# Optimization experiments

Measured on AMD Instinct MI355X. Metric: run time of the kernel, lower is better.

Reference implementation:

```python
import jax, jax.numpy as jnp
import numpy as np

D = 384      # d_model
DM = 256     # memory feature dim
DF = 1536    # dim_feedforward
EPS = 1e-5


def _layer_norm(x, g, b):
    m = jnp.mean(x, axis=-1, keepdims=True)
    v = jnp.mean(jnp.square(x - m), axis=-1, keepdims=True)
    return (x - m) * jax.lax.rsqrt(v + EPS) * g + b


def setup_inputs() -> dict:
    key = jax.random.key(0)
    ks = jax.random.split(key, 24)
    B, T, T1, Tc = 8, 2048, 2048, 2048
    s = 0.02
    inp = {
        "tgt": jax.random.normal(ks[0], (B, T, D), jnp.float32),
        "memory": jax.random.normal(ks[1], (B, T1, DM), jnp.float32),
        "a1": jnp.float32(0.5),
        "score_c": jax.random.normal(ks[2], (B, 1, Tc, T1), jnp.float32) * 0.1,
        "out_c": jax.random.normal(ks[3], (B, Tc, D), jnp.float32),
        # attention projections
        "Wq": jax.random.normal(ks[4], (D, D), jnp.float32) * s,
        "bq": jnp.zeros((D,), jnp.float32),
        "Wk": jax.random.normal(ks[5], (DM, D), jnp.float32) * s,
        "bk": jnp.zeros((D,), jnp.float32),
        "Wv": jax.random.normal(ks[6], (DM, D), jnp.float32) * s,
        "bv": jnp.zeros((D,), jnp.float32),
        "Wu": jax.random.normal(ks[7], (D, D), jnp.float32) * s,  # unknown
        "bu": jnp.zeros((D,), jnp.float32),
        "Wn": jax.random.normal(ks[8], (D, D), jnp.float32) * s,  # known
        "bn": jnp.zeros((D,), jnp.float32),
        # FFN
        "W1": jax.random.normal(ks[9], (D, DF), jnp.float32) * s,
        "b1": jnp.zeros((DF,), jnp.float32),
        "W2": jax.random.normal(ks[10], (DF, D), jnp.float32) * s,
        "b2": jnp.zeros((D,), jnp.float32),
        # LayerNorms
        "g1": jnp.ones((D,), jnp.float32),
        "be1": jnp.zeros((D,), jnp.float32),
        "g2": jnp.ones((D,), jnp.float32),
        "be2": jnp.zeros((D,), jnp.float32),
    }
    return inp


def reference(tgt, memory, a1, score_c, out_c,
              Wq, bq, Wk, bk, Wv, bv, Wu, bu, Wn, bn,
              W1, b1, W2, b2, g1, be1, g2, be2):
    # --- En_De_Attention (n_head = 1; dropout p=0 / eval mode -> identity) ---
    scale = 1.0 / jnp.sqrt(jnp.float32(D))
    q = tgt @ Wq + bq                  # [B,T,D]
    k = memory @ Wk + bk               # [B,T1,D]
    v = memory @ Wv + bv               # [B,T1,D]
    att = jnp.einsum('btd,bsd->bts', q, k) * scale            # [B,T,T1]

    unknow = tgt @ Wu + bu             # [B,T,D]
    know = out_c @ Wn + bn             # [B,Tc,D]
    score1 = jnp.einsum('btd,bcd->btc', unknow, know) * scale  # [B,T,Tc]
    mixed = jnp.einsum('btc,bcs->bts', score1, score_c[:, 0])  # [B,T,T1]

    # tt = a1 in (0,1]: blended-score branch of the original module
    score = a1 * jax.nn.softmax(mixed, axis=-1) \
          + (1.0 - a1) * jax.nn.softmax(att, axis=-1)          # [B,T,T1]
    z = jnp.einsum('bts,bsd->btd', score, v)                   # [B,T,D]

    # --- residual + norm1 ---
    x = _layer_norm(tgt + z, g1, be1)
    # --- FFN (relu) + residual + norm2 (dropout eval -> identity) ---
    ff = jax.nn.relu(x @ W1 + b1) @ W2 + b2
    out = _layer_norm(x + ff, g2, be2)
    # score2 returned with head dim, matching torch shape [B,1,T,T1]
    return out, score[:, None]
```

## Files before the change

### kernel.cpp

```cpp
#include <hip/hip_runtime.h>
#include <stdint.h>

typedef __attribute__((ext_vector_type(8))) short bf16x8;
typedef __attribute__((ext_vector_type(4))) float f32x4;

__device__ __forceinline__ short f2bf(float f) {
    union { float f; unsigned u; } v; v.f = f;
    unsigned r = v.u + 0x7fffu + ((v.u >> 16) & 1u);
    return (short)(r >> 16);
}
__device__ __forceinline__ float bf2f(short s) {
    union { unsigned u; float f; } v;
    v.u = ((unsigned)(unsigned short)s) << 16;
    return v.f;
}

__device__ __forceinline__ void gld16(const void* g, void* l) {
    auto gp = reinterpret_cast<const __attribute__((address_space(1))) unsigned int*>(
        reinterpret_cast<uintptr_t>(g));
    auto lp = reinterpret_cast<__attribute__((address_space(3))) unsigned int*>(
        reinterpret_cast<uintptr_t>(l));
    __builtin_amdgcn_global_load_lds(gp, lp, 16, 0, 0);
}

template<int OUTBF, int BIASMODE , int DORELU>
__global__ __launch_bounds__(256, 2) void gemmWide(
    const short* __restrict__ Ag, const short* __restrict__ Bg,
    void* __restrict__ Cg, const float* __restrict__ bias,
    int K, int lda, int ldb, int ldc,
    long long sA, long long sB, long long sC,
    long long dA, long long dB, long long dC, float scale)
{
    __shared__ short lds[3 * 12288];
    const int t = threadIdx.x;
    const int lane = t & 63;
    const int wave = t >> 6;
    const int wm = wave >> 1, wn = wave & 1;

    const int gx = gridDim.x, gy = gridDim.y;
    const int nwg = gx * gy * gridDim.z;
    int id = blockIdx.x + gx * (blockIdx.y + gy * blockIdx.z);
    id = (id & 7) * (nwg >> 3) + (id >> 3);
    const int bx = id % gx;
    const int by = (id / gx) % gy;
    const int bz = id / (gx * gy);
    const int zlo = bz & 7, zhi = bz >> 3;

    const long long row0 = (long long)by * 128;
    const long long col0 = (long long)bx * 256;
    const int NT = K >> 5;

    const int gk = ((t & 3) ^ ((t >> 2) & 3) ^ ((t >> 4) & 3)) * 8;
    const short* Asrc = Ag + zlo * sA + zhi * dA + (row0 + (t >> 2)) * (long long)lda + gk;
    const short* Bsrc = Bg + zlo * sB + zhi * dB + (col0 + (t >> 2)) * (long long)ldb + gk;

    const int frow = lane & 15;
    const int fcol = ((lane >> 4) ^ (frow & 3) ^ ((frow >> 2) & 3)) * 8;

    f32x4 acc[4][8] = {};

#define STG(BUF, KC) do { \
        gld16(Asrc + (KC), &lds[(BUF) * 12288 + t * 8]); \
        gld16(Asrc + (KC) + 64LL * lda, &lds[(BUF) * 12288 + 2048 + t * 8]); \
        gld16(Bsrc + (KC), &lds[(BUF) * 12288 + 4096 + t * 8]); \
        gld16(Bsrc + (KC) + 64LL * ldb, &lds[(BUF) * 12288 + 6144 + t * 8]); \
        gld16(Bsrc + (KC) + 128LL * ldb, &lds[(BUF) * 12288 + 8192 + t * 8]); \
        gld16(Bsrc + (KC) + 192LL * ldb, &lds[(BUF) * 12288 + 10240 + t * 8]); } while (0)

    STG(0, 0);
    STG(1, 32);
    asm volatile("s_waitcnt vmcnt(6)\ns_barrier" ::: "memory");

    for (int kt = 0; kt < NT; ++kt) {
        const int rb = (kt % 3) * 12288;
        bf16x8 av[4], bv[8];
#pragma unroll
        for (int m = 0; m < 4; ++m)
            av[m] = *(const bf16x8*)&lds[rb + (wm * 64 + m * 16 + frow) * 32 + fcol];
#pragma unroll
        for (int n = 0; n < 8; ++n)
            bv[n] = *(const bf16x8*)&lds[rb + 4096 + (wn * 128 + n * 16 + frow) * 32 + fcol];
        if (kt + 2 < NT) STG((kt + 2) % 3, (long long)(kt + 2) * 32);
        __builtin_amdgcn_s_setprio(1);
#pragma unroll
        for (int m = 0; m < 4; ++m)
#pragma unroll
            for (int n = 0; n < 8; ++n)
                acc[m][n] = __builtin_amdgcn_mfma_f32_16x16x32_bf16(av[m], bv[n], acc[m][n], 0, 0, 0);
        __builtin_amdgcn_s_setprio(0);
        if (kt + 1 < NT) {
            if (kt + 2 < NT) asm volatile("s_waitcnt vmcnt(6)\ns_barrier" ::: "memory");
            else             asm volatile("s_waitcnt vmcnt(0)\ns_barrier" ::: "memory");
        }
    }
#undef STG

    const int crow = (lane >> 4) * 4;
    const int ccol = lane & 15;
    const long long cz = zlo * sC + zhi * dC;
#pragma unroll
    for (int m = 0; m < 4; ++m)
#pragma unroll
        for (int n = 0; n < 8; ++n)
#pragma unroll
            for (int i = 0; i < 4; ++i) {
                long long r = row0 + wm * 64 + m * 16 + crow + i;
                long long c = col0 + wn * 128 + n * 16 + ccol;
                float v = acc[m][n][i] * scale;
                if (BIASMODE == 1) v += bias[c];
                if (DORELU) v = fmaxf(v, 0.0f);
                long long idx = cz + r * (long long)ldc + c;
                if (OUTBF) ((short*)Cg)[idx] = f2bf(v);
                else ((float*)Cg)[idx] = v;
            }
}

template<int OUTBF, int BIASMODE , int DORELU>
__global__ __launch_bounds__(256, 3) void gemm128r(
    const short* __restrict__ Ag, const short* __restrict__ Bg,
    void* __restrict__ Cg, const float* __restrict__ bias,
    int K, int lda, int ldb, int ldc,
    long long sA, long long sB, long long sC,
    long long dA, long long dB, long long dC, float scale)
{
    __shared__ short lds[3 * 8192];
    const int t = threadIdx.x;
    const int lane = t & 63;
    const int wave = t >> 6;
    const int wm = wave >> 1, wn = wave & 1;

    const int gx = gridDim.x, gy = gridDim.y;
    const int nwg = gx * gy * gridDim.z;
    int id = blockIdx.x + gx * (blockIdx.y + gy * blockIdx.z);
    id = (id & 7) * (nwg >> 3) + (id >> 3);
    const int bx = id % gx;
    const int by = (id / gx) % gy;
    const int bz = id / (gx * gy);
    const int zlo = bz & 7, zhi = bz >> 3;

    const long long row0 = (long long)by * 128;
    const long long col0 = (long long)bx * 128;
    const int NT = K >> 5;

    const int gk = ((t & 3) ^ ((t >> 2) & 3) ^ ((t >> 4) & 3)) * 8;
    const short* Asrc = Ag + zlo * sA + zhi * dA + (row0 + (t >> 2)) * (long long)lda + gk;
    const short* Bsrc = Bg + zlo * sB + zhi * dB + (col0 + (t >> 2)) * (long long)ldb + gk;

    const int frow = lane & 15;
    const int fcol = ((lane >> 4) ^ (frow & 3) ^ ((frow >> 2) & 3)) * 8;

    f32x4 acc[4][4] = {};

#define STG(BUF, KC) do { \
        gld16(Asrc + (KC), &lds[(BUF) * 8192 + t * 8]); \
        gld16(Asrc + (KC) + 64LL * lda, &lds[(BUF) * 8192 + 2048 + t * 8]); \
        gld16(Bsrc + (KC), &lds[(BUF) * 8192 + 4096 + t * 8]); \
        gld16(Bsrc + (KC) + 64LL * ldb, &lds[(BUF) * 8192 + 6144 + t * 8]); } while (0)

    STG(0, 0);
    STG(1, 32);
    asm volatile("s_waitcnt vmcnt(4)\ns_barrier" ::: "memory");

    for (int kt = 0; kt < NT; ++kt) {
        const int rb = (kt % 3) * 8192;
        bf16x8 av[4], bv[4];
#pragma unroll
        for (int m = 0; m < 4; ++m)
            av[m] = *(const bf16x8*)&lds[rb + (wm * 64 + m * 16 + frow) * 32 + fcol];
#pragma unroll
        for (int n = 0; n < 4; ++n)
            bv[n] = *(const bf16x8*)&lds[rb + 4096 + (wn * 64 + n * 16 + frow) * 32 + fcol];
        if (kt + 2 < NT) STG((kt + 2) % 3, (long long)(kt + 2) * 32);
        __builtin_amdgcn_s_setprio(1);
#pragma unroll
        for (int m = 0; m < 4; ++m)
#pragma unroll
            for (int n = 0; n < 4; ++n)
                acc[m][n] = __builtin_amdgcn_mfma_f32_16x16x32_bf16(av[m], bv[n], acc[m][n], 0, 0, 0);
        __builtin_amdgcn_s_setprio(0);
        if (kt + 1 < NT) {
            if (kt + 2 < NT) asm volatile("s_waitcnt vmcnt(4)\ns_barrier" ::: "memory");
            else             asm volatile("s_waitcnt vmcnt(0)\ns_barrier" ::: "memory");
        }
    }
#undef STG

    const int crow = (lane >> 4) * 4;
    const int ccol = lane & 15;
    const long long cz = zlo * sC + zhi * dC;
#pragma unroll
    for (int m = 0; m < 4; ++m)
#pragma unroll
        for (int n = 0; n < 4; ++n)
#pragma unroll
            for (int i = 0; i < 4; ++i) {
                long long r = row0 + wm * 64 + m * 16 + crow + i;
                long long c = col0 + wn * 64 + n * 16 + ccol;
                float v = acc[m][n][i] * scale;
                if (BIASMODE == 1) v += bias[c];
                if (BIASMODE == 2) v += bias[r];
                if (DORELU) v = fmaxf(v, 0.0f);
                long long idx = cz + r * (long long)ldc + c;
                if (OUTBF) ((short*)Cg)[idx] = f2bf(v);
                else ((float*)Cg)[idx] = v;
            }
}

#define RD_A(RB, M, KS) (*(const bf16x8*)&lds[(RB) + (wm * 64 + (M) * 16 + frow) * 64 + \
        ((((KS) << 2) | fq) ^ (frow & 7)) * 8])
#define RD_B(RB, Nn, KS) (*(const bf16x8*)&lds[(RB) + 8192 + (wn * 64 + (Nn) * 16 + frow) * 64 + \
        ((((KS) << 2) | fq) ^ (frow & 7)) * 8])

__global__ __launch_bounds__(256, 2) void gemm128pz(
    const short* __restrict__ A1, const short* __restrict__ B1, short* __restrict__ C1,
    const float* __restrict__ bias1, int K1, int lda1, int ldb1, int ldc1,
    long long sB1, long long sC1,
    const short* __restrict__ A2, const short* __restrict__ B2, short* __restrict__ C2,
    const float* __restrict__ bias2, int K2, int lda2, int ldb2, int ldc2,
    long long sB2, long long sC2)
{
    __shared__ short lds[2 * 16384];
    const int t = threadIdx.x;
    const int lane = t & 63;
    const int wave = t >> 6;
    const int wm = wave >> 1, wn = wave & 1;

    const int gx = gridDim.x, gy = gridDim.y;
    const int nwg = gx * gy * gridDim.z;
    int id = blockIdx.x + gx * (blockIdx.y + gy * blockIdx.z);
    id = (id & 7) * (nwg >> 3) + (id >> 3);
    const int bx = id % gx;
    const int by = (id / gx) % gy;
    const int bz = id / (gx * gy);

    const bool sel = bz >= 8;
    const int zz = bz & 7;
    const short* Ag = sel ? A2 : A1;
    const short* Bg = sel ? B2 : B1;
    short* Cg = sel ? C2 : C1;
    const float* bias = sel ? bias2 : bias1;
    const int K = sel ? K2 : K1;
    const int lda = sel ? lda2 : lda1;
    const int ldb = sel ? ldb2 : ldb1;
    const int ldc = sel ? ldc2 : ldc1;
    const long long sB = sel ? sB2 : sB1;
    const long long sC = sel ? sC2 : sC1;

    const long long row0 = (long long)by * 128;
    const long long col0 = (long long)bx * 128;
    const int NT = K >> 6;

    const int srow = t >> 3;
    const int gk = ((t & 7) ^ (srow & 7)) * 8;
    const short* Asrc = Ag + (row0 + srow) * (long long)lda + gk;
    const short* Bsrc = Bg + (long long)zz * sB + (col0 + srow) * (long long)ldb + gk;

    const int frow = lane & 15;
    const int fq = lane >> 4;

    f32x4 acc[4][4] = {};

#define STAGE_A(WB, KC) do { _Pragma("unroll") \
        for (int r = 0; r < 4; ++r) \
            gld16(Asrc + (KC) + (long long)r * 32 * lda, &lds[(WB) + t * 8 + r * 2048]); } while (0)
#define STAGE_B(WB, KC) do { _Pragma("unroll") \
        for (int r = 0; r < 4; ++r) \
            gld16(Bsrc + (KC) + (long long)r * 32 * ldb, &lds[(WB) + 8192 + t * 8 + r * 2048]); } while (0)

    STAGE_A(0, 0);
    STAGE_B(0, 0);
    asm volatile("s_waitcnt vmcnt(0)\ns_barrier" ::: "memory");

    for (int kt = 0; kt < NT; ++kt) {
        const int rb = (kt & 1) << 14;
        const int wb = ((kt + 1) & 1) << 14;
        const bool st = (kt + 1) < NT;
        const long long kc = (long long)(kt + 1) << 6;

        bf16x8 av[4], bv[4];

#pragma unroll
        for (int m = 0; m < 4; ++m) av[m] = RD_A(rb, m, 0);
#pragma unroll
        for (int n = 0; n < 4; ++n) bv[n] = RD_B(rb, n, 0);
        if (st) STAGE_A(wb, kc);
        asm volatile("s_barrier" ::: "memory");
        __builtin_amdgcn_s_setprio(1);
#pragma unroll
        for (int m = 0; m < 4; ++m)
#pragma unroll
            for (int n = 0; n < 4; ++n)
                acc[m][n] = __builtin_amdgcn_mfma_f32_16x16x32_bf16(av[m], bv[n], acc[m][n], 0, 0, 0);
        __builtin_amdgcn_s_setprio(0);
        asm volatile("s_barrier" ::: "memory");

#pragma unroll
        for (int m = 0; m < 4; ++m) av[m] = RD_A(rb, m, 1);
#pragma unroll
        for (int n = 0; n < 4; ++n) bv[n] = RD_B(rb, n, 1);
        if (st) STAGE_B(wb, kc);
        asm volatile("s_barrier" ::: "memory");
        __builtin_amdgcn_s_setprio(1);
#pragma unroll
        for (int m = 0; m < 4; ++m)
#pragma unroll
            for (int n = 0; n < 4; ++n)
                acc[m][n] = __builtin_amdgcn_mfma_f32_16x16x32_bf16(av[m], bv[n], acc[m][n], 0, 0, 0);
        __builtin_amdgcn_s_setprio(0);
        if (st) asm volatile("s_waitcnt vmcnt(0)\ns_barrier" ::: "memory");
        else    asm volatile("s_barrier" ::: "memory");
    }
#undef STAGE_A
#undef STAGE_B

    const int crow = (lane >> 4) * 4;
    const int ccol = lane & 15;
    const long long cz = (long long)zz * sC;
#pragma unroll
    for (int m = 0; m < 4; ++m)
#pragma unroll
        for (int n = 0; n < 4; ++n)
#pragma unroll
            for (int i = 0; i < 4; ++i) {
                long long r = row0 + wm * 64 + m * 16 + crow + i;
                long long c = col0 + wn * 64 + n * 16 + ccol;
                float v = acc[m][n][i] + bias[r];
                Cg[cz + r * (long long)ldc + c] = f2bf(v);
            }
}
#undef RD_A
#undef RD_B

__global__ __launch_bounds__(256) void cast_all(
    const float* __restrict__ tgt, const float* __restrict__ mem, const float* __restrict__ outc,
    const float* __restrict__ bq, const float* __restrict__ bu,
    short* __restrict__ tgtb, short* __restrict__ memb, short* __restrict__ outcb,
    float* __restrict__ qubias)
{
    const long long R1 = 1572864;
    const long long R2 = R1 + 1048576;
    const long long R3 = R2 + 1572864;
    const long long R4 = R3 + 192;
    long long i = (long long)blockIdx.x * 256 + threadIdx.x;
    const float* in; short* out; long long j;
    if (i < R1) { in = tgt; out = tgtb; j = i; }
    else if (i < R2) { in = mem; out = memb; j = i - R1; }
    else if (i < R3) { in = outc; out = outcb; j = i - R2; }
    else if (i < R4) {
        j = i - R3;
        ((float4*)qubias)[j] = (j < 96) ? ((const float4*)bq)[j] : ((const float4*)bu)[j - 96];
        return;
    } else return;
    float4 v = ((const float4*)in)[j];
    short4 o;
    o.x = f2bf(v.x); o.y = f2bf(v.y); o.z = f2bf(v.z); o.w = f2bf(v.w);
    ((short4*)out)[j] = o;
}

__global__ __launch_bounds__(256) void transpose_all(
    const float* __restrict__ Wq, const float* __restrict__ Wk, const float* __restrict__ Wv,
    const float* __restrict__ Wu, const float* __restrict__ Wn,
    const float* __restrict__ W1, const float* __restrict__ W2,
    short* __restrict__ WquT, short* __restrict__ WkT, short* __restrict__ WvT,
    short* __restrict__ WnT, short* __restrict__ W1T, short* __restrict__ W2T)
{
    __shared__ float tile[64][65];
    int b = blockIdx.x;
    const float* in; short* out; int R, C, local;
    if (b < 36)       { in = Wq; out = WquT;          R = 384;  C = 384;  local = b; }
    else if (b < 60)  { in = Wk; out = WkT;           R = 256;  C = 384;  local = b - 36; }
    else if (b < 84)  { in = Wv; out = WvT;           R = 256;  C = 384;  local = b - 60; }
    else if (b < 120) { in = Wu; out = WquT + 147456; R = 384;  C = 384;  local = b - 84; }
    else if (b < 156) { in = Wn; out = WnT;           R = 384;  C = 384;  local = b - 120; }
    else if (b < 300) { in = W1; out = W1T;           R = 384;  C = 1536; local = b - 156; }
    else              { in = W2; out = W2T;           R = 1536; C = 384;  local = b - 300; }
    const int nbx = C >> 6;
    const int r0 = (local / nbx) * 64, c0 = (local % nbx) * 64;
    const int lr = threadIdx.x >> 6, lc = threadIdx.x & 63;
#pragma unroll
    for (int i = 0; i < 16; ++i) {
        int r = lr * 16 + i;
        tile[r][lc] = in[(long long)(r0 + r) * C + c0 + lc];
    }
    __syncthreads();
#pragma unroll
    for (int i = 0; i < 16; ++i) {
        int r = lr * 16 + i;
        out[(long long)(c0 + r) * R + r0 + lc] = f2bf(tile[lc][r]);
    }
}

__global__ __launch_bounds__(256) void transpose_cast(
    const float* __restrict__ in, short* __restrict__ out,
    int R, int C, long long sIn, long long sOut)
{
    __shared__ float tile[64][65];
    const long long zi = (long long)blockIdx.z * sIn;
    const long long zo = (long long)blockIdx.z * sOut;
    const int r0 = blockIdx.y * 64, c0 = blockIdx.x * 64;
    const int lr = threadIdx.x >> 6, lc = threadIdx.x & 63;
#pragma unroll
    for (int i = 0; i < 16; ++i) {
        int r = lr * 16 + i;
        tile[r][lc] = in[zi + (long long)(r0 + r) * C + c0 + lc];
    }
    __syncthreads();
#pragma unroll
    for (int i = 0; i < 16; ++i) {
        int r = lr * 16 + i;
        out[zo + (long long)(c0 + r) * R + r0 + lc] = f2bf(tile[lc][r]);
    }
}

__global__ __launch_bounds__(256) void softmax_blend(
    const short* __restrict__ attb, const short* __restrict__ mixb,
    const float* __restrict__ a1p,
    float* __restrict__ outF, short* __restrict__ outB)
{
    const int S = 2048;
    const long long row = blockIdx.x;
    const short* ar = attb + row * S;
    const short* mr = mixb + row * S;
    const int t = threadIdx.x;
    const int wave = t >> 6;

    bf16x8 a8 = *(const bf16x8*)&ar[t * 8];
    bf16x8 m8 = *(const bf16x8*)&mr[t * 8];
    float av[8], mv[8];
#pragma unroll
    for (int i = 0; i < 8; ++i) { av[i] = bf2f(a8[i]); mv[i] = bf2f(m8[i]); }

    float amax = av[0], mmax = mv[0];
#pragma unroll
    for (int i = 1; i < 8; ++i) { amax = fmaxf(amax, av[i]); mmax = fmaxf(mmax, mv[i]); }
#pragma unroll
    for (int o = 32; o; o >>= 1) {
        amax = fmaxf(amax, __shfl_xor(amax, o));
        mmax = fmaxf(mmax, __shfl_xor(mmax, o));
    }
    __shared__ float red[2][4];
    if ((t & 63) == 0) { red[0][wave] = amax; red[1][wave] = mmax; }
    __syncthreads();
    amax = fmaxf(fmaxf(red[0][0], red[0][1]), fmaxf(red[0][2], red[0][3]));
    mmax = fmaxf(fmaxf(red[1][0], red[1][1]), fmaxf(red[1][2], red[1][3]));

    float asum = 0.f, msum = 0.f;
#pragma unroll
    for (int i = 0; i < 8; ++i) {
        av[i] = __expf(av[i] - amax); asum += av[i];
        mv[i] = __expf(mv[i] - mmax); msum += mv[i];
    }
#pragma unroll
    for (int o = 32; o; o >>= 1) {
        asum += __shfl_xor(asum, o);
        msum += __shfl_xor(msum, o);
    }
    __shared__ float red2[2][4];
    if ((t & 63) == 0) { red2[0][wave] = asum; red2[1][wave] = msum; }
    __syncthreads();
    asum = red2[0][0] + red2[0][1] + red2[0][2] + red2[0][3];
    msum = red2[1][0] + red2[1][1] + red2[1][2] + red2[1][3];

    const float a1 = a1p[0];
    const float wm = a1 / msum;
    const float wa = (1.0f - a1) / asum;

    float o0[8];
    bf16x8 ob;
#pragma unroll
    for (int i = 0; i < 8; ++i) {
        float s = wm * mv[i] + wa * av[i];
        o0[i] = s;
        ob[i] = f2bf(s);
    }
    float4 f0, f1;
    f0.x = o0[0]; f0.y = o0[1]; f0.z = o0[2]; f0.w = o0[3];
    f1.x = o0[4]; f1.y = o0[5]; f1.z = o0[6]; f1.w = o0[7];
    *(float4*)&outF[row * S + t * 8] = f0;
    *(float4*)&outF[row * S + t * 8 + 4] = f1;
    *(bf16x8*)&outB[row * S + t * 8] = ob;
}

template<int WRITE_BF, int TWO_Y>
__global__ __launch_bounds__(256) void ln_kernel(
    const float* __restrict__ X, const float* __restrict__ Yr,
    const float* __restrict__ Y2,
    const float* __restrict__ g, const float* __restrict__ be,
    float* __restrict__ outF, short* __restrict__ outB)
{
    const int Dm = 384;
    const int wave = threadIdx.x >> 6, lane = threadIdx.x & 63;
    const long long row = (long long)blockIdx.x * 4 + wave;
    const float* x = X + row * Dm;
    const float* y = Yr + row * Dm;
    const float* y2 = TWO_Y ? (Y2 + row * Dm) : nullptr;
    float h[6];
    float s = 0.f, s2 = 0.f;
#pragma unroll
    for (int j = 0; j < 6; ++j) {
        int c = j * 64 + lane;
        h[j] = x[c] + y[c];
        if (TWO_Y) h[j] += y2[c];
        s += h[j]; s2 += h[j] * h[j];
    }
#pragma unroll
    for (int o = 32; o; o >>= 1) { s += __shfl_xor(s, o); s2 += __shfl_xor(s2, o); }
    const float mean = s * (1.0f / 384.0f);
    const float var = s2 * (1.0f / 384.0f) - mean * mean;
    const float rstd = rsqrtf(var + 1e-5f);
#pragma unroll
    for (int j = 0; j < 6; ++j) {
        int c = j * 64 + lane;
        float v = (h[j] - mean) * rstd * g[c] + be[c];
        outF[row * Dm + c] = v;
        if (WRITE_BF) outB[row * Dm + c] = f2bf(v);
    }
}

extern "C" void kernel_launch(void* const* d_in, const int* in_sizes, int n_in,
                              void* d_out, int out_size, void* d_ws, size_t ws_size,
                              hipStream_t stream) {
    const float* tgt     = (const float*)d_in[0];
    const float* memory  = (const float*)d_in[1];
    const float* a1      = (const float*)d_in[2];
    const float* score_c = (const float*)d_in[3];
    const float* out_c   = (const float*)d_in[4];
    const float* Wq = (const float*)d_in[5];  const float* bq = (const float*)d_in[6];
    const float* Wk = (const float*)d_in[7];  const float* bk = (const float*)d_in[8];
    const float* Wv = (const float*)d_in[9];  const float* bv = (const float*)d_in[10];
    const float* Wu = (const float*)d_in[11]; const float* bu = (const float*)d_in[12];
    const float* Wn = (const float*)d_in[13]; const float* bn = (const float*)d_in[14];
    const float* W1 = (const float*)d_in[15]; const float* b1 = (const float*)d_in[16];
    const float* W2 = (const float*)d_in[17]; const float* b2 = (const float*)d_in[18];
    const float* g1 = (const float*)d_in[19]; const float* be1 = (const float*)d_in[20];
    const float* g2 = (const float*)d_in[21]; const float* be2 = (const float*)d_in[22];

    const long long BT = 16384;
    const long long S2 = 2048LL * 2048;
    const long long PB = 2048LL * 384;
    char* ws = (char*)d_ws;
    size_t off = 0;
    auto A_ = [&](size_t b) { size_t r = off; off += (b + 255) & ~(size_t)255; return r; };

    const size_t oTgtB  = A_(BT * 384 * 2);
    const size_t oMemB  = A_(BT * 256 * 2);
    const size_t oOutcB = A_(BT * 384 * 2);
    const size_t oWquT  = A_(768 * 384 * 2);
    const size_t oWnT   = A_(384 * 384 * 2);
    const size_t oWkT   = A_(384 * 256 * 2);
    const size_t oWvT   = A_(384 * 256 * 2);
    const size_t oW1T   = A_(1536 * 384 * 2);
    const size_t oW2T   = A_(384 * 1536 * 2);
    const size_t oQUb   = A_(768 * 4);
    const size_t oQU    = A_(16 * PB * 2);
    const size_t oKP    = A_(16 * PB * 2);
    const size_t oVT    = A_(8LL * 384 * 2048 * 2);
    const size_t oJ     = A_(8 * S2 * 2);
    const size_t oKr    = A_(8 * S2 * 2);
    const size_t oAM    = A_(16 * S2 * 2);
    const size_t oX     = A_(BT * 384 * 4);
    const size_t oXB    = A_(BT * 384 * 2);

    short* tgt_bf  = (short*)(ws + oTgtB);
    short* mem_bf  = (short*)(ws + oMemB);
    short* outc_bf = (short*)(ws + oOutcB);
    short* WquT = (short*)(ws + oWquT);
    short* WnT  = (short*)(ws + oWnT);
    short* WkT  = (short*)(ws + oWkT);
    short* WvT  = (short*)(ws + oWvT);
    short* W1T  = (short*)(ws + oW1T);
    short* W2T  = (short*)(ws + oW2T);
    float* qu_bias = (float*)(ws + oQUb);
    short* qu_bf  = (short*)(ws + oQU);
    short* k_bf   = (short*)(ws + oKP);
    short* Pt_bf  = k_bf + 8 * PB;
    short* vT_bf  = (short*)(ws + oVT);
    short* score_bf = (short*)(ws + oJ);
    short* scoreCt  = (short*)(ws + oKr);
    float* z0_f     = (float*)(ws + oKr);
    float* z1_f     = z0_f + 6291456;
    short* knoT_bf  = (short*)(ws + oAM);
    short* att_bf   = (short*)(ws + oAM);
    short* mix_bf   = att_bf + 8 * S2;
    short* h_bf     = (short*)(ws + oAM);
    float* ff_f     = (float*)(ws + oAM + 8 * S2 * 2);
    float* x_f  = (float*)(ws + oX);
    short* x_bf = (short*)(ws + oXB);

    float* outMain = (float*)d_out;
    float* outScore = (float*)d_out + 6291456;

    const float SC = 0.05103103630798288f;
    dim3 blk(256);

    cast_all<<<16385, blk, 0, stream>>>(tgt, memory, out_c, bq, bu,
                                        tgt_bf, mem_bf, outc_bf, qu_bias);
    transpose_all<<<444, blk, 0, stream>>>(Wq, Wk, Wv, Wu, Wn, W1, W2,
                                           WquT, WkT, WvT, WnT, W1T, W2T);
    transpose_cast<<<dim3(32, 32, 8), blk, 0, stream>>>(score_c, scoreCt, 2048, 2048, S2, S2);

    gemmWide<1, 1, 0><<<dim3(3, 128, 1), blk, 0, stream>>>(
        tgt_bf, WquT, qu_bf, qu_bias, 384, 384, 384, 768, 0, 0, 0, 0, 0, 0, 1.0f);
    gemm128r<1, 1, 0><<<dim3(3, 128, 1), blk, 0, stream>>>(
        mem_bf, WkT, k_bf, bk, 256, 256, 256, 384, 0, 0, 0, 0, 0, 0, 1.0f);
    gemm128pz<<<dim3(16, 3, 16), blk, 0, stream>>>(
        WvT, mem_bf, vT_bf, bv, 256, 256, 256, 2048, 2048LL * 256, PB,
        WnT, outc_bf, knoT_bf, bn, 384, 384, 384, 2048, PB, PB);
    gemm128r<1, 0, 0><<<dim3(3, 16, 8), blk, 0, stream>>>(
        scoreCt, knoT_bf, Pt_bf, nullptr, 2048, 2048, 2048, 384,
        S2, PB, PB, 0, 0, 0, 1.0f);
    gemmWide<1, 0, 0><<<dim3(8, 16, 16), blk, 0, stream>>>(
        qu_bf, k_bf, att_bf, nullptr, 384, 768, 384, 2048,
        2048LL * 768, PB, S2, 384, 8 * PB, 8 * S2, SC);
    softmax_blend<<<16384, blk, 0, stream>>>(att_bf, mix_bf, a1, outScore, score_bf);
    gemm128r<0, 0, 0><<<dim3(3, 16, 16), blk, 0, stream>>>(
        score_bf, vT_bf, z0_f, nullptr, 1024, 2048, 2048, 384,
        S2, PB, PB, 1024, 1024, 6291456, 1.0f);
    ln_kernel<1, 1><<<4096, blk, 0, stream>>>(tgt, z0_f, z1_f, g1, be1, x_f, x_bf);
    gemmWide<1, 1, 1><<<dim3(6, 128, 1), blk, 0, stream>>>(
        x_bf, W1T, h_bf, b1, 384, 384, 384, 1536, 0, 0, 0, 0, 0, 0, 1.0f);
    gemm128r<0, 1, 0><<<dim3(3, 128, 1), blk, 0, stream>>>(
        h_bf, W2T, ff_f, b2, 1536, 1536, 1536, 384, 0, 0, 0, 0, 0, 0, 1.0f);
    ln_kernel<0, 0><<<4096, blk, 0, stream>>>(x_f, ff_f, nullptr, g2, be2, outMain, nullptr);
}
```

Measured before the change: 446.9 us.

## Split-K the Pt and FFN2 GEMMs and switch the QU projection to gemm128r

The Pt = score_c^T·know GEMM and the FFN down-projection are split along K into two fp32 partial outputs, which doubles the number of blocks for these low-grid GEMMs. The Pt partials are summed and cast to bf16 by a new combine kernel. The FFN partials and the b2 bias are summed inside the second LayerNorm through new template flags. The fused Q/U projection also moves from gemmWide to gemm128r with twice as many column tiles. The cost is extra fp32 partial traffic and one more kernel launch.

```diff
diff --git a/kernel.cpp b/kernel.cpp
--- a/kernel.cpp
+++ b/kernel.cpp
@@ -330,6 +330,20 @@
 }
 #undef RD_A
 #undef RD_B
+
+__global__ __launch_bounds__(256) void combine_bf(
+    const float* __restrict__ p, long long half, short* __restrict__ out)
+{
+    long long i = ((long long)blockIdx.x * 256 + threadIdx.x) * 4;
+    if (i + 3 < half) {
+        float4 a = *(const float4*)&p[i];
+        float4 b = *(const float4*)&p[i + half];
+        short4 o;
+        o.x = f2bf(a.x + b.x); o.y = f2bf(a.y + b.y);
+        o.z = f2bf(a.z + b.z); o.w = f2bf(a.w + b.w);
+        *(short4*)&out[i] = o;
+    }
+}
 
 __global__ __launch_bounds__(256) void cast_all(
     const float* __restrict__ tgt, const float* __restrict__ mem, const float* __restrict__ outc,
@@ -481,10 +495,10 @@
     *(bf16x8*)&outB[row * S + t * 8] = ob;
 }
 
-template<int WRITE_BF, int TWO_Y>
+template<int WRITE_BF, int TWO_Y, int CBIAS>
 __global__ __launch_bounds__(256) void ln_kernel(
     const float* __restrict__ X, const float* __restrict__ Yr,
-    const float* __restrict__ Y2,
+    const float* __restrict__ Y2, const float* __restrict__ cb,
     const float* __restrict__ g, const float* __restrict__ be,
     float* __restrict__ outF, short* __restrict__ outB)
 {
@@ -501,6 +515,7 @@
         int c = j * 64 + lane;
         h[j] = x[c] + y[c];
         if (TWO_Y) h[j] += y2[c];
+        if (CBIAS) h[j] += cb[c];
         s += h[j]; s2 += h[j] * h[j];
     }
 #pragma unroll
@@ -580,10 +595,12 @@
     float* z0_f     = (float*)(ws + oKr);
     float* z1_f     = z0_f + 6291456;
     short* knoT_bf  = (short*)(ws + oAM);
+    float* ptH_f    = (float*)(ws + oAM + 16LL * 1024 * 1024);
     short* att_bf   = (short*)(ws + oAM);
     short* mix_bf   = att_bf + 8 * S2;
     short* h_bf     = (short*)(ws + oAM);
-    float* ff_f     = (float*)(ws + oAM + 8 * S2 * 2);
+    float* ff0_f    = (float*)(ws + oAM + 8 * S2 * 2);
+    float* ff1_f    = ff0_f + 6291456;
     float* x_f  = (float*)(ws + oX);
     short* x_bf = (short*)(ws + oXB);
 
@@ -599,16 +616,17 @@
                                            WquT, WkT, WvT, WnT, W1T, W2T);
     transpose_cast<<<dim3(32, 32, 8), blk, 0, stream>>>(score_c, scoreCt, 2048, 2048, S2, S2);
 
-    gemmWide<1, 1, 0><<<dim3(3, 128, 1), blk, 0, stream>>>(
+    gemm128r<1, 1, 0><<<dim3(6, 128, 1), blk, 0, stream>>>(
         tgt_bf, WquT, qu_bf, qu_bias, 384, 384, 384, 768, 0, 0, 0, 0, 0, 0, 1.0f);
     gemm128r<1, 1, 0><<<dim3(3, 128, 1), blk, 0, stream>>>(
         mem_bf, WkT, k_bf, bk, 256, 256, 256, 384, 0, 0, 0, 0, 0, 0, 1.0f);
     gemm128pz<<<dim3(16, 3, 16), blk, 0, stream>>>(
         WvT, mem_bf, vT_bf, bv, 256, 256, 256, 2048, 2048LL * 256, PB,
         WnT, outc_bf, knoT_bf, bn, 384, 384, 384, 2048, PB, PB);
-    gemm128r<1, 0, 0><<<dim3(3, 16, 8), blk, 0, stream>>>(
-        scoreCt, knoT_bf, Pt_bf, nullptr, 2048, 2048, 2048, 384,
-        S2, PB, PB, 0, 0, 0, 1.0f);
+    gemm128r<0, 0, 0><<<dim3(3, 16, 16), blk, 0, stream>>>(
+        scoreCt, knoT_bf, ptH_f, nullptr, 1024, 2048, 2048, 384,
+        S2, PB, PB, 1024, 1024, 6291456, 1.0f);
+    combine_bf<<<6144, blk, 0, stream>>>(ptH_f, 6291456, Pt_bf);
     gemmWide<1, 0, 0><<<dim3(8, 16, 16), blk, 0, stream>>>(
         qu_bf, k_bf, att_bf, nullptr, 384, 768, 384, 2048,
         2048LL * 768, PB, S2, 384, 8 * PB, 8 * S2, SC);
@@ -616,10 +634,11 @@
     gemm128r<0, 0, 0><<<dim3(3, 16, 16), blk, 0, stream>>>(
         score_bf, vT_bf, z0_f, nullptr, 1024, 2048, 2048, 384,
         S2, PB, PB, 1024, 1024, 6291456, 1.0f);
-    ln_kernel<1, 1><<<4096, blk, 0, stream>>>(tgt, z0_f, z1_f, g1, be1, x_f, x_bf);
+    ln_kernel<1, 1, 0><<<4096, blk, 0, stream>>>(tgt, z0_f, z1_f, nullptr, g1, be1, x_f, x_bf);
     gemmWide<1, 1, 1><<<dim3(6, 128, 1), blk, 0, stream>>>(
         x_bf, W1T, h_bf, b1, 384, 384, 384, 1536, 0, 0, 0, 0, 0, 0, 1.0f);
-    gemm128r<0, 1, 0><<<dim3(3, 128, 1), blk, 0, stream>>>(
-        h_bf, W2T, ff_f, b2, 1536, 1536, 1536, 384, 0, 0, 0, 0, 0, 0, 1.0f);
-    ln_kernel<0, 0><<<4096, blk, 0, stream>>>(x_f, ff_f, nullptr, g2, be2, outMain, nullptr);
-}
+    gemm128r<0, 0, 0><<<dim3(3, 128, 2), blk, 0, stream>>>(
+        h_bf, W2T, ff0_f, nullptr, 768, 1536, 1536, 384,
+        768, 768, 6291456, 0, 0, 0, 1.0f);
+    ln_kernel<0, 1, 1><<<4096, blk, 0, stream>>>(x_f, ff0_f, ff1_f, b2, g2, be2, outMain, nullptr);
+}
```

New measurement: 455.2 us. No clear change (+1.9%).
